# Optimization experiments

Measured on AMD Instinct MI355X. Metric: run time of the kernel, lower is better.

Reference implementation:

```python
import jax, jax.numpy as jnp
import numpy as np

B, S, D = 2, 2048, 2048
H, KV, HD = 32, 8, 64
REP = H // KV  # 4


def setup_inputs() -> dict:
    key = jax.random.key(0)
    ks = jax.random.split(key, 5)
    x = jax.random.normal(ks[0], (B, S, D), jnp.float32)
    # Llama rope frequencies: theta=10000, pairs of adjacent dims
    inv_freq = 1.0 / (10000.0 ** (np.arange(0, HD, 2, dtype=np.float64) / HD))  # [HD/2]
    ang = np.outer(np.arange(S, dtype=np.float64), inv_freq)  # [S, HD/2]
    freqs_cis = jnp.asarray(np.stack([np.cos(ang), np.sin(ang)], axis=-1), jnp.float32)  # [S, HD/2, 2]
    wq = jax.random.normal(ks[1], (H * HD, D), jnp.float32) * 0.02
    wk = jax.random.normal(ks[2], (KV * HD, D), jnp.float32) * 0.02
    wv = jax.random.normal(ks[3], (KV * HD, D), jnp.float32) * 0.02
    wo = jax.random.normal(ks[4], (D, H * HD), jnp.float32) * 0.02
    return {"x": x, "freqs_cis": freqs_cis, "wq": wq, "wk": wk, "wv": wv, "wo": wo}


def _apply_rope(t, cos, sin):
    # t: [B,S,nh,HD]; cos/sin: [S,HD/2]; complex multiply on adjacent pairs
    b, s, nh, hd = t.shape
    t2 = t.reshape(b, s, nh, hd // 2, 2)
    tr, ti = t2[..., 0], t2[..., 1]
    c = cos[None, :, None, :]
    sn = sin[None, :, None, :]
    out = jnp.stack([tr * c - ti * sn, tr * sn + ti * c], axis=-1)
    return out.reshape(b, s, nh, hd)


def reference(x, freqs_cis, wq, wk, wv, wo):
    # QKV projections (torch Linear: y = x @ W.T)
    q = jnp.einsum('bsd,ed->bse', x, wq).reshape(B, S, H, HD)
    k = jnp.einsum('bsd,ed->bse', x, wk).reshape(B, S, KV, HD)
    v = jnp.einsum('bsd,ed->bse', x, wv).reshape(B, S, KV, HD)
    cos, sin = freqs_cis[..., 0], freqs_cis[..., 1]
    q = _apply_rope(q, cos, sin)
    k = _apply_rope(k, cos, sin)
    # GQA without materializing repeated K/V: group query heads by KV head
    qg = q.reshape(B, S, KV, REP, HD)
    scale = 1.0 / jnp.sqrt(jnp.asarray(HD, q.dtype))
    scores = jnp.einsum('bsgrd,btgd->bgrst', qg, k) * scale  # [B,KV,REP,S,S]
    causal = jnp.tril(jnp.ones((S, S), bool))
    scores = jnp.where(causal, scores, -jnp.inf)
    p = jax.nn.softmax(scores, axis=-1)
    o = jnp.einsum('bgrst,btgd->bsgrd', p, v).reshape(B, S, H * HD)
    return jnp.einsum('bse,de->bsd', o, wo)
```

## Files before the change

kernel.cpp:

```cpp
#include <hip/hip_runtime.h>
#include <cstdint>
#include <cstddef>

#define B_ 2
#define S_ 2048
#define D_ 2048
#define H_ 32
#define KV_ 8
#define HD_ 64
#define M_ (B_*S_)
#define EQ_ (H_*HD_)
#define EK_ (KV_*HD_)

typedef unsigned short u16;
typedef __attribute__((ext_vector_type(8))) short s16x8;
typedef __attribute__((ext_vector_type(4))) float f32x4;

#define QSCALE 0.18033688011112042f
#define EXPOFF 15.869645449778564f

#if __has_builtin(__builtin_amdgcn_exp2f)
#define EXP2(x) __builtin_amdgcn_exp2f(x)
#else
#define EXP2(x) __expf((x) * 0.6931471805599453f)
#endif

__device__ __forceinline__ u16 f2bf(float f) {
  unsigned u = __float_as_uint(f);
  u += 0x7fffu + ((u >> 16) & 1u);
  return (u16)(u >> 16);
}
__device__ __forceinline__ unsigned pk2(float a, float b) {
  unsigned ua = __float_as_uint(a) + 0x8000u;
  unsigned ub = __float_as_uint(b) + 0x8000u;
  return __builtin_amdgcn_perm(ub, ua, 0x07060302);
}
__device__ __forceinline__ f32x4 mfma16(s16x8 a, s16x8 b, f32x4 c) {
  return __builtin_amdgcn_mfma_f32_16x16x32_bf16(a, b, c, 0, 0, 0);
}
__device__ __forceinline__ void gl_lds16(const void* g, void* l) {
  __builtin_amdgcn_global_load_lds(
      (const __attribute__((address_space(1))) void*)g,
      (__attribute__((address_space(3))) void*)l, 16, 0, 0);
}

__global__ void cast_all(const float4* __restrict__ x, const float4* __restrict__ wq,
                         const float4* __restrict__ wk, const float4* __restrict__ wv,
                         const float4* __restrict__ wo, ushort4* __restrict__ dst) {
  int i = blockIdx.x * 256 + threadIdx.x;
  const float4* src; int off;
  if (i < 2097152)      { src = x;  off = i; }
  else if (i < 3145728) { src = wq; off = i - 2097152; }
  else if (i < 3407872) { src = wk; off = i - 3145728; }
  else if (i < 3670016) { src = wv; off = i - 3407872; }
  else                  { src = wo; off = i - 3670016; }
  float4 v = src[off];
  ushort4 r;
  r.x = f2bf(v.x); r.y = f2bf(v.y); r.z = f2bf(v.z); r.w = f2bf(v.w);
  dst[i] = r;
}

__global__ __launch_bounds__(256)
void gemm_qkv(const u16* __restrict__ A, const u16* __restrict__ Bw,
              u16* __restrict__ qb, u16* __restrict__ kb, u16* __restrict__ vtb,
              const float* __restrict__ fc) {
  __shared__ __align__(16) u16 As[128 * 64];
  __shared__ __align__(16) u16 Bs[96 * 64];
  const int tid  = threadIdx.x;
  const int lane = tid & 63;
  const int wave = tid >> 6;
  const int m0 = blockIdx.y * 128;
  const int n0 = blockIdx.x * 96;
  const int wm = (wave >> 1) * 64;
  const int wn = (wave & 1) * 48;
  const int l15 = lane & 15;
  const int quad = lane >> 4;

  f32x4 acc[4][3] = {};

  for (int k0 = 0; k0 < D_; k0 += 64) {
    #pragma unroll
    for (int rr = 0; rr < 4; ++rr) {
      int c = tid + rr * 256;
      int row = c >> 3;
      int ksrc = ((c & 7) ^ (row & 7)) * 8;
      gl_lds16(A + (size_t)(m0 + row) * D_ + k0 + ksrc, &As[c * 8]);
    }
    #pragma unroll
    for (int rr = 0; rr < 3; ++rr) {
      int c = tid + rr * 256;
      int row = c >> 3;
      int ksrc = ((c & 7) ^ (row & 7)) * 8;
      gl_lds16(Bw + (size_t)(n0 + row) * D_ + k0 + ksrc, &Bs[c * 8]);
    }
    __syncthreads();

    #pragma unroll
    for (int kc = 0; kc < 2; ++kc) {
      s16x8 af[4], bfr[3];
      #pragma unroll
      for (int mi = 0; mi < 4; ++mi) {
        int row = wm + mi * 16 + l15;
        af[mi]  = *(const s16x8*)&As[row * 64 + (((kc * 4 + quad) ^ (row & 7)) * 8)];
      }
      #pragma unroll
      for (int ni = 0; ni < 3; ++ni) {
        int row = wn + ni * 16 + l15;
        bfr[ni] = *(const s16x8*)&Bs[row * 64 + (((kc * 4 + quad) ^ (row & 7)) * 8)];
      }
      #pragma unroll
      for (int mi = 0; mi < 4; ++mi)
        #pragma unroll
        for (int ni = 0; ni < 3; ++ni)
          acc[mi][ni] = mfma16(af[mi], bfr[ni], acc[mi][ni]);
    }
    __syncthreads();
  }

  const float sg = (l15 & 1) ? 1.f : -1.f;
  #pragma unroll
  for (int mi = 0; mi < 4; ++mi) {
    #pragma unroll
    for (int ni = 0; ni < 3; ++ni) {
      const int col = n0 + wn + ni * 16 + l15;
      if (col < 2560) {
        const bool isQ = (col < 2048);
        u16* dst = isQ ? qb : kb;
        const int ncol0 = isQ ? 0 : 2048;
        const int ndim  = isQ ? EQ_ : EK_;
        const float scale = isQ ? QSCALE : 1.0f;
        const int ip = (col & 63) >> 1;
        #pragma unroll
        for (int r = 0; r < 4; ++r) {
          int row = m0 + wm + mi * 16 + quad * 4 + r;
          const float* fr = fc + (size_t)(row & (S_ - 1)) * 64;
          float c  = fr[ip * 2];
          float sn = fr[ip * 2 + 1];
          float v = acc[mi][ni][r];
          float p = __shfl_xor(v, 1, 64);
          float o = (v * c + sg * (p * sn)) * scale;
          dst[(size_t)row * ndim + col - ncol0] = f2bf(o);
        }
      } else {
        const int vcol = col - 2560;
        uint2 w;
        w.x = pk2(acc[mi][ni][0], acc[mi][ni][1]);
        w.y = pk2(acc[mi][ni][2], acc[mi][ni][3]);
        *(uint2*)(vtb + (size_t)vcol * M_ + m0 + wm + mi * 16 + quad * 4) = w;
      }
    }
  }
}

__global__ __launch_bounds__(256)
void gemm_o(const u16* __restrict__ A, const u16* __restrict__ Bw, float* __restrict__ C,
            int Ndim, int Kdim) {
  __shared__ __align__(16) u16 As[64 * 64];
  __shared__ __align__(16) u16 Bs[128 * 64];
  const int tid  = threadIdx.x;
  const int lane = tid & 63;
  const int wave = tid >> 6;
  const int m0 = blockIdx.y * 64;
  const int n0 = blockIdx.x * 128;
  const int wm = (wave >> 1) * 32;
  const int wn = (wave & 1) * 64;
  const int l15 = lane & 15;
  const int quad = lane >> 4;

  f32x4 acc[2][4] = {};

  for (int k0 = 0; k0 < Kdim; k0 += 64) {
    #pragma unroll
    for (int rr = 0; rr < 2; ++rr) {
      int c = tid + rr * 256;
      int row = c >> 3;
      int ksrc = ((c & 7) ^ (row & 7)) * 8;
      gl_lds16(A + (size_t)(m0 + row) * Kdim + k0 + ksrc, &As[c * 8]);
    }
    #pragma unroll
    for (int rr = 0; rr < 4; ++rr) {
      int c = tid + rr * 256;
      int row = c >> 3;
      int ksrc = ((c & 7) ^ (row & 7)) * 8;
      gl_lds16(Bw + (size_t)(n0 + row) * Kdim + k0 + ksrc, &Bs[c * 8]);
    }
    __syncthreads();

    #pragma unroll
    for (int kc = 0; kc < 2; ++kc) {
      s16x8 af[2], bfr[4];
      #pragma unroll
      for (int mi = 0; mi < 2; ++mi) {
        int row = wm + mi * 16 + l15;
        af[mi]  = *(const s16x8*)&As[row * 64 + (((kc * 4 + quad) ^ (row & 7)) * 8)];
      }
      #pragma unroll
      for (int ni = 0; ni < 4; ++ni) {
        int row = wn + ni * 16 + l15;
        bfr[ni] = *(const s16x8*)&Bs[row * 64 + (((kc * 4 + quad) ^ (row & 7)) * 8)];
      }
      #pragma unroll
      for (int mi = 0; mi < 2; ++mi)
        #pragma unroll
        for (int ni = 0; ni < 4; ++ni)
          acc[mi][ni] = mfma16(af[mi], bfr[ni], acc[mi][ni]);
    }
    __syncthreads();
  }

  #pragma unroll
  for (int mi = 0; mi < 2; ++mi) {
    #pragma unroll
    for (int r = 0; r < 4; ++r) {
      int row = m0 + wm + mi * 16 + quad * 4 + r;
      size_t base = (size_t)row * Ndim + n0 + wn;
      #pragma unroll
      for (int ni = 0; ni < 4; ++ni)
        C[base + ni * 16 + l15] = acc[mi][ni][r];
    }
  }
}

__global__ __launch_bounds__(256, 4)
void flash_attn(const u16* __restrict__ qb, const u16* __restrict__ kb,
                const u16* __restrict__ vtb, u16* __restrict__ ob) {
  const int bx = blockIdx.x;
  const int h  = blockIdx.y;
  const int b  = blockIdx.z;
  const int g  = h >> 2;
  const int tid  = threadIdx.x;
  const int lane = tid & 63;
  const int wave = tid >> 6;
  const int l15  = lane & 15;
  const int quad = lane >> 4;
  const int kq   = quad * 8;

  const int Tlo = bx, Thi = 31 - bx;
  const int n_lo = Tlo + 1, n_hi = Thi + 1;
  const int rL = Tlo * 64 + wave * 16;
  const int rH = Thi * 64 + wave * 16;
  const int rowL = rL + l15;
  const int rowH = rH + l15;

  __shared__ __align__(16) u16 Ks[8 * 512];
  __shared__ __align__(16) u16 Vs[8 * 512];
  __shared__ __align__(16) u16 Pl[4][2][16 * 72];

  u16* PbL = &Pl[wave][0][0];
  u16* PbH = &Pl[wave][1][0];

  const u16* qpL = qb + (size_t)(b * S_ + rL + l15) * EQ_ + h * HD_;
  const u16* qpH = qb + (size_t)(b * S_ + rH + l15) * EQ_ + h * HD_;
  s16x8 qL0 = *(const s16x8*)(qpL + kq);
  s16x8 qL1 = *(const s16x8*)(qpL + 32 + kq);
  s16x8 qH0 = *(const s16x8*)(qpH + kq);
  s16x8 qH1 = *(const s16x8*)(qpH + 32 + kq);

  f32x4 OL[4] = {}, OH[4] = {};
  float sumL = 0.f, sumH = 0.f;

  const int sw = wave & 1;
  const bool doK = (wave < 2);

  for (int kt = 0; kt < n_hi; ++kt) {
    const int t0 = kt * 64;

    if (doK) {
      const u16* src = kb + (size_t)(b * S_ + t0 + lane) * EK_ + g * HD_;
      #pragma unroll
      for (int r = 0; r < 4; ++r) {
        int i = sw * 4 + r;
        gl_lds16(src + i * 8, &Ks[i * 512 + lane * 8]);
      }
    } else {
      const u16* src = vtb + (size_t)(g * HD_ + lane) * M_ + b * S_ + t0;
      #pragma unroll
      for (int r = 0; r < 4; ++r) {
        int i = sw * 4 + r;
        gl_lds16(src + i * 8, &Vs[i * 512 + lane * 8]);
      }
    }
    __syncthreads();

    const bool do_lo = (kt < n_lo);
    const bool mH = (kt == n_hi - 1);
    const bool mL = (kt == n_lo - 1);

    #pragma unroll
    for (int ts = 0; ts < 4; ++ts) {
      s16x8 k0 = *(const s16x8*)&Ks[quad * 512 + (ts * 16 + l15) * 8];
      s16x8 k1 = *(const s16x8*)&Ks[(4 + quad) * 512 + (ts * 16 + l15) * 8];
      const int tb = t0 + ts * 16 + quad * 4;
      {
        f32x4 s = {};
        s = mfma16(k0, qH0, s);
        s = mfma16(k1, qH1, s);
        if (mH) {
          #pragma unroll
          for (int r = 0; r < 4; ++r) if (tb + r > rowH) s[r] = -1e30f;
        }
        float p0 = EXP2(s[0] - EXPOFF), p1 = EXP2(s[1] - EXPOFF);
        float p2 = EXP2(s[2] - EXPOFF), p3 = EXP2(s[3] - EXPOFF);
        sumH += (p0 + p1) + (p2 + p3);
        uint2 w; w.x = pk2(p0, p1); w.y = pk2(p2, p3);
        *(uint2*)&PbH[l15 * 72 + ts * 16 + quad * 4] = w;
      }
      if (do_lo) {
        f32x4 s = {};
        s = mfma16(k0, qL0, s);
        s = mfma16(k1, qL1, s);
        if (mL) {
          #pragma unroll
          for (int r = 0; r < 4; ++r) if (tb + r > rowL) s[r] = -1e30f;
        }
        float p0 = EXP2(s[0] - EXPOFF), p1 = EXP2(s[1] - EXPOFF);
        float p2 = EXP2(s[2] - EXPOFF), p3 = EXP2(s[3] - EXPOFF);
        sumL += (p0 + p1) + (p2 + p3);
        uint2 w; w.x = pk2(p0, p1); w.y = pk2(p2, p3);
        *(uint2*)&PbL[l15 * 72 + ts * 16 + quad * 4] = w;
      }
    }

    s16x8 pH0 = *(const s16x8*)&PbH[l15 * 72 + kq];
    s16x8 pH1 = *(const s16x8*)&PbH[l15 * 72 + 32 + kq];
    s16x8 pL0 = {}, pL1 = {};
    if (do_lo) {
      pL0 = *(const s16x8*)&PbL[l15 * 72 + kq];
      pL1 = *(const s16x8*)&PbL[l15 * 72 + 32 + kq];
    }

    #pragma unroll
    for (int df = 0; df < 4; ++df) {
      s16x8 v0 = *(const s16x8*)&Vs[quad * 512 + (df * 16 + l15) * 8];
      s16x8 v1 = *(const s16x8*)&Vs[(4 + quad) * 512 + (df * 16 + l15) * 8];
      OH[df] = mfma16(v1, pH1, mfma16(v0, pH0, OH[df]));
      if (do_lo) OL[df] = mfma16(v1, pL1, mfma16(v0, pL0, OL[df]));
    }
    __syncthreads();
  }

  sumH += __shfl_xor(sumH, 16, 64); sumH += __shfl_xor(sumH, 32, 64);
  sumL += __shfl_xor(sumL, 16, 64); sumL += __shfl_xor(sumL, 32, 64);
  float invH = 1.f / sumH, invL = 1.f / sumL;

  {
    u16* op = ob + (size_t)(b * S_ + rowH) * EQ_ + h * HD_;
    #pragma unroll
    for (int df = 0; df < 4; ++df) {
      uint2 w;
      w.x = pk2(OH[df][0] * invH, OH[df][1] * invH);
      w.y = pk2(OH[df][2] * invH, OH[df][3] * invH);
      *(uint2*)(op + df * 16 + quad * 4) = w;
    }
  }
  {
    u16* op = ob + (size_t)(b * S_ + rowL) * EQ_ + h * HD_;
    #pragma unroll
    for (int df = 0; df < 4; ++df) {
      uint2 w;
      w.x = pk2(OL[df][0] * invL, OL[df][1] * invL);
      w.y = pk2(OL[df][2] * invL, OL[df][3] * invL);
      *(uint2*)(op + df * 16 + quad * 4) = w;
    }
  }
}

extern "C" void kernel_launch(void* const* d_in, const int* in_sizes, int n_in,
                              void* d_out, int out_size, void* d_ws, size_t ws_size,
                              hipStream_t stream) {
  (void)in_sizes; (void)n_in; (void)out_size; (void)ws_size;
  const float* x  = (const float*)d_in[0];
  const float* fc = (const float*)d_in[1];
  const float* wq = (const float*)d_in[2];
  const float* wk = (const float*)d_in[3];
  const float* wv = (const float*)d_in[4];
  const float* wo = (const float*)d_in[5];
  float* out = (float*)d_out;
  char* ws = (char*)d_ws;

  u16* xb  = (u16*)(ws);
  u16* wqb = (u16*)(ws + 16777216);
  u16* wob = (u16*)(ws + 29360128);
  u16* qb  = (u16*)(ws + 37748736);
  u16* kb  = (u16*)(ws + 54525952);
  u16* vtb = (u16*)(ws + 58720256);
  u16* ob  = (u16*)(ws + 62914560);

  cast_all<<<18432, 256, 0, stream>>>((const float4*)x, (const float4*)wq,
                                      (const float4*)wk, (const float4*)wv,
                                      (const float4*)wo, (ushort4*)ws);

  gemm_qkv<<<dim3(32, 32), 256, 0, stream>>>(xb, wqb, qb, kb, vtb, fc);

  flash_attn<<<dim3(16, 32, 2), 256, 0, stream>>>(qb, kb, vtb, ob);

  gemm_o<<<dim3(16, 64), 256, 0, stream>>>(ob, wob, out, D_, EQ_);
}
```

Baseline: 300.7 us.

## Prefetch next K/V tile into registers during attention compute

The attention loop now issues global loads for the next 64-row K/V tile into registers before computing the current tile. After the compute and a barrier, those registers are written to LDS, followed by a second barrier. This is meant to hide global memory latency behind the MFMA work. In exchange it adds register pressure, an extra barrier per iteration, and replaces direct global-to-LDS loads with a register round-trip.

```diff
diff --git a/kernel.cpp b/kernel.cpp
--- a/kernel.cpp
+++ b/kernel.cpp
@@ -262,25 +262,35 @@
   const int sw = wave & 1;
   const bool doK = (wave < 2);
 
+  const u16* stbase;
+  size_t     tstride;
+  u16*       ldst;
+  if (doK) {
+    stbase  = kb + (size_t)(b * S_ + lane) * EK_ + g * HD_ + sw * 32;
+    tstride = (size_t)64 * EK_;
+    ldst    = &Ks[sw * 4 * 512 + lane * 8];
+  } else {
+    stbase  = vtb + (size_t)(g * HD_ + lane) * M_ + b * S_ + sw * 32;
+    tstride = 64;
+    ldst    = &Vs[sw * 4 * 512 + lane * 8];
+  }
+
+  #pragma unroll
+  for (int r = 0; r < 4; ++r)
+    gl_lds16(stbase + r * 8, ldst + r * 512);
+  __syncthreads();
+
   for (int kt = 0; kt < n_hi; ++kt) {
     const int t0 = kt * 64;
 
-    if (doK) {
-      const u16* src = kb + (size_t)(b * S_ + t0 + lane) * EK_ + g * HD_;
-      #pragma unroll
-      for (int r = 0; r < 4; ++r) {
-        int i = sw * 4 + r;
-        gl_lds16(src + i * 8, &Ks[i * 512 + lane * 8]);
-      }
-    } else {
-      const u16* src = vtb + (size_t)(g * HD_ + lane) * M_ + b * S_ + t0;
-      #pragma unroll
-      for (int r = 0; r < 4; ++r) {
-        int i = sw * 4 + r;
-        gl_lds16(src + i * 8, &Vs[i * 512 + lane * 8]);
-      }
-    }
-    __syncthreads();
+    const bool pf = (kt + 1 < n_hi);
+    uint4 st[4] = {};
+    if (pf) {
+      const u16* src = stbase + (size_t)(kt + 1) * tstride;
+      #pragma unroll
+      for (int r = 0; r < 4; ++r)
+        st[r] = *(const uint4*)(src + r * 8);
+    }
 
     const bool do_lo = (kt < n_lo);
     const bool mH = (kt == n_hi - 1);
@@ -337,6 +347,13 @@
       if (do_lo) OL[df] = mfma16(v1, pL1, mfma16(v0, pL0, OL[df]));
     }
     __syncthreads();
+
+    if (pf) {
+      #pragma unroll
+      for (int r = 0; r < 4; ++r)
+        *(uint4*)(ldst + r * 512) = st[r];
+    }
+    __syncthreads();
   }
 
   sumH += __shfl_xor(sumH, 16, 64); sumH += __shfl_xor(sumH, 32, 64);
```

Result: slower. 454.3 us (+51.1%).
